# Kernel optimization log

Hardware: AMD Instinct MI355X
Metric: run time of the kernel (lower is better)

The kernel has to match this reference:

```python
import jax, jax.numpy as jnp
import numpy as np

H = 16  # heads
K_POLY = 3  # K from init


def setup_inputs() -> dict:
    key = jax.random.key(0)
    ks = jax.random.split(key, 6)
    B, N, D = 4, 1024, 1024
    s = 1.0 / np.sqrt(D)
    return {
        "x": jax.random.normal(ks[0], (B, N, D), jnp.float32),
        "Wq": jax.random.normal(ks[1], (D, D), jnp.float32) * s,
        "bq": jnp.zeros((D,), jnp.float32),
        "Wk": jax.random.normal(ks[2], (D, D), jnp.float32) * s,
        "bk": jnp.zeros((D,), jnp.float32),
        "Wv": jax.random.normal(ks[3], (D, D), jnp.float32) * s,
        "bv": jnp.zeros((D,), jnp.float32),
        "Wo": jax.random.normal(ks[4], (D, D), jnp.float32) * s,
        "bo": jnp.zeros((D,), jnp.float32),
        "w0": jnp.zeros((H,), jnp.float32),
        "w1": jnp.ones((H,), jnp.float32),
        "wK": jnp.zeros((H,), jnp.float32),
    }


def reference(x, Wq, bq, Wk, bk, Wv, bv, Wo, bo, w0, w1, wK):
    B, N, D = x.shape
    d = D // H
    # projections -> [B, H, N, d]
    def proj(W, b):
        return (x @ W + b).reshape(B, N, H, d).transpose(0, 2, 1, 3)
    q = proj(Wq, bq)
    k = proj(Wk, bk)
    v = proj(Wv, bv)
    att = jax.nn.softmax(jnp.einsum('bhnd,bhmd->bhnm', q, k) / jnp.sqrt(jnp.float32(d)), axis=-1)
    att2 = jnp.einsum('bhnm,bhmk->bhnk', att, att)  # att @ att
    attK = att + (K_POLY - 1) * (att2 - att)
    eye = jnp.eye(N, dtype=x.dtype)  # [N, N]
    gf = (w0[None, :, None, None] * eye[None, None]
          + w1[None, :, None, None] * att
          + wK[None, :, None, None] * attK)
    out = jnp.einsum('bhnm,bhmd->bhnd', gf, v)  # [B, H, N, d]
    out = out.transpose(0, 2, 1, 3).reshape(B, N, D)
    return out @ Wo + bo
```

## Files before the change

### kernel.cpp

```cpp
#include <hip/hip_runtime.h>

typedef unsigned short u16;
typedef unsigned int u32;
typedef __attribute__((ext_vector_type(8))) short short8;
typedef __attribute__((ext_vector_type(4))) float f32x4;

__device__ __forceinline__ u16 f2bf(float f) {
  union { float f; u32 u; } c; c.f = f;
  u32 u = c.u;
  u += 0x7fffu + ((u >> 16) & 1u);
  return (u16)(u >> 16);
}
__device__ __forceinline__ float bf2f(u16 h) {
  union { u32 u; float f; } c; c.u = ((u32)h) << 16;
  return c.f;
}

#define GLDS16(g, l)                                                          \
  __builtin_amdgcn_global_load_lds(                                           \
      (const __attribute__((address_space(1))) u32*)(g),                      \
      (__attribute__((address_space(3))) u32*)(l), 16, 0, 0)

#define EXP_SCALE 0.18033688011112042f

__global__ __launch_bounds__(256) void k_cast_x(const float* __restrict__ x,
                                                u16* __restrict__ xb) {
  int i = blockIdx.x * 256 + threadIdx.x;
  float4 v = ((const float4*)x)[i];
  short4 s;
  s.x = (short)f2bf(v.x); s.y = (short)f2bf(v.y);
  s.z = (short)f2bf(v.z); s.w = (short)f2bf(v.w);
  *(short4*)(xb + (size_t)i * 4) = s;
}

__global__ __launch_bounds__(256) void k_trans_w(
    const float* __restrict__ W0, const float* __restrict__ W1,
    const float* __restrict__ W2, const float* __restrict__ W3,
    u16* __restrict__ T0, u16* __restrict__ T1, u16* __restrict__ T2,
    u16* __restrict__ T3) {
  const float* W = blockIdx.z == 0 ? W0 : blockIdx.z == 1 ? W1 : blockIdx.z == 2 ? W2 : W3;
  u16* T = blockIdx.z == 0 ? T0 : blockIdx.z == 1 ? T1 : blockIdx.z == 2 ? T2 : T3;
  __shared__ float tile[32][33];
  int r0 = blockIdx.y * 32, c0 = blockIdx.x * 32;
  int tid = threadIdx.x;
  for (int i = tid; i < 1024; i += 256) {
    int r = i >> 5, c = i & 31;
    tile[r][c] = W[(size_t)(r0 + r) * 1024 + c0 + c];
  }
  __syncthreads();
  for (int i = tid; i < 1024; i += 256) {
    int r = i >> 5, c = i & 31;
    T[(size_t)(c0 + r) * 1024 + r0 + c] = f2bf(tile[c][r]);
  }
}

__global__ __launch_bounds__(512, 2) void k_proj(
    const u16* __restrict__ xb, const u16* __restrict__ WqT,
    const u16* __restrict__ WkT, const u16* __restrict__ WvT,
    const float* __restrict__ bq, const float* __restrict__ bk,
    const float* __restrict__ bv, u16* __restrict__ qh, u16* __restrict__ kh,
    u16* __restrict__ vh, u16* __restrict__ vT) {
  __shared__ __align__(16) u16 As[3 * 256 * 32];
  __shared__ __align__(16) u16 Bs[3 * 256 * 32];
  const int li = blockIdx.x;
  const int cx = li & 7, j = li >> 3;
  const int g = cx * 24 + j;
  const int which = g >> 6;
  const int rem = g & 63;
  const int n0 = (rem >> 4) * 256;
  const int m0 = (rem & 15) * 256;
  const u16* Ag = xb + (size_t)m0 * 1024;
  const u16* Bg = (which == 0 ? WqT : which == 1 ? WkT : WvT) + (size_t)n0 * 1024;
  const float* bias = which == 0 ? bq : which == 1 ? bk : bv;
  const int tid = threadIdx.x, lane = tid & 63, wid = tid >> 6;
  const int wm = wid >> 2, wn = wid & 3, fr = lane & 15, fg = lane >> 4;

  f32x4 acc[8][4];
#pragma unroll
  for (int i = 0; i < 8; ++i)
#pragma unroll
    for (int jj = 0; jj < 4; ++jj) acc[i][jj] = f32x4{0.f, 0.f, 0.f, 0.f};

  auto stage = [&](int t, int slot) {
    u16* as = As + slot * 8192;
    u16* bs = Bs + slot * 8192;
#pragma unroll
    for (int L = 0; L < 2; ++L) {
      int q = L * 512 + tid;
      int row = q >> 2, c = q & 3;
      GLDS16(Ag + (size_t)row * 1024 + t * 32 + c * 8, as + q * 8);
    }
#pragma unroll
    for (int L = 0; L < 2; ++L) {
      int q = L * 512 + tid;
      int row = q >> 2, c = q & 3;
      GLDS16(Bg + (size_t)row * 1024 + t * 32 + c * 8, bs + q * 8);
    }
  };
  auto compute = [&](int slot) {
    const u16* as = As + slot * 8192;
    const u16* bs = Bs + slot * 8192;
    short8 bf_[4];
#pragma unroll
    for (int jj = 0; jj < 4; ++jj) {
      int row = wn * 64 + jj * 16 + fr;
      bf_[jj] = *(const short8*)(bs + row * 32 + fg * 8);
    }
    short8 af_[8];
#pragma unroll
    for (int i = 0; i < 8; ++i) {
      int row = wm * 128 + i * 16 + fr;
      af_[i] = *(const short8*)(as + row * 32 + fg * 8);
    }
#pragma unroll
    for (int i = 0; i < 8; ++i)
#pragma unroll
      for (int jj = 0; jj < 4; ++jj)
        acc[i][jj] = __builtin_amdgcn_mfma_f32_16x16x32_bf16(af_[i], bf_[jj],
                                                             acc[i][jj], 0, 0, 0);
  };

  const int NS = 32;
  stage(0, 0);
  stage(1, 1);
  int cs = 0, ss = 2;
  for (int t = 0; t + 2 < NS; ++t) {
    asm volatile("s_waitcnt vmcnt(4) lgkmcnt(0)" ::: "memory");
    __builtin_amdgcn_s_barrier();
    asm volatile("" ::: "memory");
    stage(t + 2, ss);
    compute(cs);
    cs = cs == 2 ? 0 : cs + 1;
    ss = ss == 2 ? 0 : ss + 1;
  }
  asm volatile("s_waitcnt vmcnt(4) lgkmcnt(0)" ::: "memory");
  __builtin_amdgcn_s_barrier();
  asm volatile("" ::: "memory");
  compute(cs);
  cs = cs == 2 ? 0 : cs + 1;
  asm volatile("s_waitcnt vmcnt(0) lgkmcnt(0)" ::: "memory");
  __builtin_amdgcn_s_barrier();
  asm volatile("" ::: "memory");
  compute(cs);

#pragma unroll
  for (int f = 0; f < 8; ++f)
#pragma unroll
    for (int j2 = 0; j2 < 4; ++j2) {
      int n = n0 + wn * 64 + j2 * 16 + fr;
      float bb = bias[n];
      int h = n >> 6, dc = n & 63;
#pragma unroll
      for (int r = 0; r < 4; ++r) {
        int m = m0 + wm * 128 + f * 16 + fg * 4 + r;
        int b = m >> 10, nr = m & 1023;
        int z = b * 16 + h;
        float val = acc[f][j2][r] + bb;
        u16 bv16 = f2bf(val);
        if (which == 0) {
          qh[((size_t)z * 1024 + nr) * 64 + dc] = bv16;
        } else if (which == 1) {
          kh[((size_t)z * 1024 + nr) * 64 + dc] = bv16;
        } else {
          vh[((size_t)z * 1024 + nr) * 64 + dc] = bv16;
          vT[((size_t)z * 64 + dc) * 1024 + nr] = bv16;
        }
      }
    }
}

__device__ __forceinline__ void core128x64_p3(const u16* __restrict__ A,
                                              const u16* __restrict__ Bt, int K,
                                              f32x4 (&acc)[2][4], u16* As,
                                              u16* Bs) {
  const int tid = threadIdx.x;
  const int lane = tid & 63;
  const int w = tid >> 6;
  const int fr = lane & 15, fg = lane >> 4;
  const int sr = tid >> 2, sc = (tid & 3) * 8;
#pragma unroll
  for (int i = 0; i < 2; ++i)
#pragma unroll
    for (int j = 0; j < 4; ++j) acc[i][j] = f32x4{0.f, 0.f, 0.f, 0.f};

  auto stage = [&](int t, int slot) {
    u16* as = As + slot * 4096;
    u16* bs = Bs + slot * 2048;
    const int k0 = t * 32 + sc;
    GLDS16(A + (size_t)sr * K + k0, as + tid * 8);
    GLDS16(A + (size_t)(sr + 64) * K + k0, as + (256 + tid) * 8);
    GLDS16(Bt + (size_t)sr * K + k0, bs + tid * 8);
  };
  auto compute = [&](int slot) {
    const u16* as = As + slot * 4096;
    const u16* bs = Bs + slot * 2048;
    short8 af[2], bfv[4];
#pragma unroll
    for (int i = 0; i < 2; ++i)
      af[i] = *(const short8*)(as + (w * 32 + i * 16 + fr) * 32 + fg * 8);
#pragma unroll
    for (int j = 0; j < 4; ++j)
      bfv[j] = *(const short8*)(bs + (j * 16 + fr) * 32 + fg * 8);
#pragma unroll
    for (int i = 0; i < 2; ++i)
#pragma unroll
      for (int j = 0; j < 4; ++j)
        acc[i][j] = __builtin_amdgcn_mfma_f32_16x16x32_bf16(af[i], bfv[j],
                                                            acc[i][j], 0, 0, 0);
  };

  const int NS = K / 32;
  stage(0, 0);
  stage(1, 1);
  int cs = 0, ss = 2;
  for (int t = 0; t + 2 < NS; ++t) {
    asm volatile("s_waitcnt vmcnt(3) lgkmcnt(0)" ::: "memory");
    __builtin_amdgcn_s_barrier();
    asm volatile("" ::: "memory");
    stage(t + 2, ss);
    compute(cs);
    cs = cs == 2 ? 0 : cs + 1;
    ss = ss == 2 ? 0 : ss + 1;
  }
  asm volatile("s_waitcnt vmcnt(3) lgkmcnt(0)" ::: "memory");
  __builtin_amdgcn_s_barrier();
  asm volatile("" ::: "memory");
  compute(cs);
  cs = cs == 2 ? 0 : cs + 1;
  asm volatile("s_waitcnt vmcnt(0) lgkmcnt(0)" ::: "memory");
  __builtin_amdgcn_s_barrier();
  asm volatile("" ::: "memory");
  compute(cs);
}

__global__ __launch_bounds__(256) void k_pass1(
    const u16* __restrict__ qh, const u16* __restrict__ kh,
    const u16* __restrict__ vT, u16* __restrict__ P1T,
    u16* __restrict__ P1h, float* __restrict__ mlinv) {
  __shared__ __align__(16) u16 Ks[64 * 64];
  __shared__ __align__(16) u16 Vs[64 * 64];
  __shared__ __align__(16) u16 Ps[4][16 * 64];
  const int li = blockIdx.x + 16 * blockIdx.y;
  const int cx = li & 7, jb = li >> 3;
  const int z = cx * 8 + (jb >> 4);
  const int m0 = (jb & 15) * 64;
  const int tid = threadIdx.x, lane = tid & 63, w = tid >> 6;
  const int fr = lane & 15, fg = lane >> 4;
  const int row0 = m0 + w * 16;
  const u16* qbase = qh + (size_t)z * 65536;
  const u16* kbase = kh + (size_t)z * 65536;
  const u16* vbase = vT + (size_t)z * 65536;
  u16* myP = &Ps[w][0];

  short8 qf[2];
#pragma unroll
  for (int kc = 0; kc < 2; ++kc)
    qf[kc] = *(const short8*)(qbase + (size_t)(row0 + fr) * 64 + (kc * 4 + fg) * 8);

  f32x4 o[4];
  float rs[4];
#pragma unroll
  for (int ct = 0; ct < 4; ++ct) o[ct] = f32x4{0.f, 0.f, 0.f, 0.f};
#pragma unroll
  for (int r = 0; r < 4; ++r) rs[r] = 0.f;

  for (int t = 0; t < 16; ++t) {
    const int kv0 = t * 64;
#pragma unroll
    for (int it = 0; it < 2; ++it) {
      int idx = it * 256 + tid;
      int row = idx >> 3, cc = idx & 7;
      GLDS16(kbase + (size_t)(kv0 + row) * 64 + ((cc ^ (row & 7)) * 8),
             Ks + idx * 8);
      GLDS16(vbase + (size_t)row * 1024 + kv0 + ((cc ^ (row & 7)) * 8),
             Vs + idx * 8);
    }
    __syncthreads();
#pragma unroll
    for (int ct = 0; ct < 4; ++ct) {
      int krow = ct * 16 + fr;
      short8 k0 = *(const short8*)(Ks + krow * 64 + ((fg ^ (krow & 7)) * 8));
      short8 k1 = *(const short8*)(Ks + krow * 64 + (((4 + fg) ^ (krow & 7)) * 8));
      f32x4 s = __builtin_amdgcn_mfma_f32_16x16x32_bf16(
          qf[0], k0, f32x4{0.f, 0.f, 0.f, 0.f}, 0, 0, 0);
      s = __builtin_amdgcn_mfma_f32_16x16x32_bf16(qf[1], k1, s, 0, 0, 0);
      int pcol = ct * 16 + fr;
      int cc = pcol >> 3;
#pragma unroll
      for (int r = 0; r < 4; ++r) {
        float e = __builtin_exp2f(s[r] * EXP_SCALE);
        rs[r] += e;
        int prow = fg * 4 + r;
        myP[prow * 64 + ((cc ^ (prow & 7)) * 8) + (pcol & 7)] = f2bf(e);
      }
    }
    asm volatile("s_waitcnt lgkmcnt(0)" ::: "memory");
    short8 p0 = *(const short8*)(myP + fr * 64 + ((fg ^ (fr & 7)) * 8));
    short8 p1 = *(const short8*)(myP + fr * 64 + (((4 + fg) ^ (fr & 7)) * 8));
#pragma unroll
    for (int ct = 0; ct < 4; ++ct) {
      int vrow = ct * 16 + fr;
      short8 v0 = *(const short8*)(Vs + vrow * 64 + ((fg ^ (vrow & 7)) * 8));
      short8 v1 = *(const short8*)(Vs + vrow * 64 + (((4 + fg) ^ (vrow & 7)) * 8));
      o[ct] = __builtin_amdgcn_mfma_f32_16x16x32_bf16(p0, v0, o[ct], 0, 0, 0);
      o[ct] = __builtin_amdgcn_mfma_f32_16x16x32_bf16(p1, v1, o[ct], 0, 0, 0);
    }
    __syncthreads();
  }
#pragma unroll
  for (int off = 1; off < 16; off <<= 1)
#pragma unroll
    for (int r = 0; r < 4; ++r) rs[r] += __shfl_xor(rs[r], off, 64);
  float linv[4];
#pragma unroll
  for (int r = 0; r < 4; ++r) linv[r] = 1.f / rs[r];
#pragma unroll
  for (int ct = 0; ct < 4; ++ct) {
    union { u16 u[4]; short4 s4; } pk;
#pragma unroll
    for (int r = 0; r < 4; ++r) {
      u16 b_ = f2bf(o[ct][r] * linv[r]);
      pk.u[r] = b_;
      myP[(fg * 4 + r) * 64 + ct * 16 + fr] = b_;
    }
    *(short4*)(P1T + ((size_t)z * 64 + ct * 16 + fr) * 1024 + row0 + fg * 4) =
        pk.s4;
  }
  asm volatile("s_waitcnt lgkmcnt(0)" ::: "memory");
  {
    int r_ = lane >> 2;
#pragma unroll
    for (int ch2 = 0; ch2 < 2; ++ch2) {
      int ch = (lane & 3) * 2 + ch2;
      int4 vv = *(const int4*)(myP + r_ * 64 + ch * 8);
      *(int4*)(P1h + ((size_t)z * 1024 + row0 + r_) * 64 + ch * 8) = vv;
    }
  }
  if (fr == 0) {
#pragma unroll
    for (int r = 0; r < 4; ++r)
      mlinv[(size_t)z * 1024 + row0 + fg * 4 + r] = linv[r];
  }
}

__global__ __launch_bounds__(256) void k_pass2(
    const u16* __restrict__ qh, const u16* __restrict__ kh,
    const u16* __restrict__ P1T, const u16* __restrict__ vh,
    const u16* __restrict__ P1h, const float* __restrict__ mlinv,
    const float* __restrict__ w0, const float* __restrict__ w1,
    const float* __restrict__ wK, u16* __restrict__ OH) {
  __shared__ __align__(16) u16 Ks[64 * 64];
  __shared__ __align__(16) u16 Ts[64 * 64];
  __shared__ __align__(16) u16 Ps[4][16 * 64];
  const int li = blockIdx.x + 16 * blockIdx.y;
  const int cx = li & 7, jb = li >> 3;
  const int z = cx * 8 + (jb >> 4);
  const int m0 = (jb & 15) * 64;
  const int tid = threadIdx.x, lane = tid & 63, w = tid >> 6;
  const int fr = lane & 15, fg = lane >> 4;
  const int row0 = m0 + w * 16;
  const int h = z & 15, b = z >> 4;
  const float cw0 = w0[h], cw1 = w1[h] - wK[h], cw2 = 2.f * wK[h];
  const u16* qbase = qh + (size_t)z * 65536;
  const u16* kbase = kh + (size_t)z * 65536;
  const u16* tbase = P1T + (size_t)z * 65536;
  u16* myP = &Ps[w][0];

  short8 qf[2];
#pragma unroll
  for (int kc = 0; kc < 2; ++kc)
    qf[kc] = *(const short8*)(qbase + (size_t)(row0 + fr) * 64 + (kc * 4 + fg) * 8);
  float lrow[4];
#pragma unroll
  for (int r = 0; r < 4; ++r)
    lrow[r] = mlinv[(size_t)z * 1024 + row0 + fg * 4 + r];
  f32x4 o[4];
#pragma unroll
  for (int ct = 0; ct < 4; ++ct) o[ct] = f32x4{0.f, 0.f, 0.f, 0.f};

  for (int t = 0; t < 16; ++t) {
    const int kv0 = t * 64;
#pragma unroll
    for (int it = 0; it < 2; ++it) {
      int idx = it * 256 + tid;
      int row = idx >> 3, cc = idx & 7;
      GLDS16(kbase + (size_t)(kv0 + row) * 64 + ((cc ^ (row & 7)) * 8),
             Ks + idx * 8);
      GLDS16(tbase + (size_t)row * 1024 + kv0 + ((cc ^ (row & 7)) * 8),
             Ts + idx * 8);
    }
    __syncthreads();
#pragma unroll
    for (int ct = 0; ct < 4; ++ct) {
      int krow = ct * 16 + fr;
      short8 k0 = *(const short8*)(Ks + krow * 64 + ((fg ^ (krow & 7)) * 8));
      short8 k1 = *(const short8*)(Ks + krow * 64 + (((4 + fg) ^ (krow & 7)) * 8));
      f32x4 s = __builtin_amdgcn_mfma_f32_16x16x32_bf16(
          qf[0], k0, f32x4{0.f, 0.f, 0.f, 0.f}, 0, 0, 0);
      s = __builtin_amdgcn_mfma_f32_16x16x32_bf16(qf[1], k1, s, 0, 0, 0);
      int pcol = ct * 16 + fr;
      int cc = pcol >> 3;
#pragma unroll
      for (int r = 0; r < 4; ++r) {
        float p = __builtin_exp2f(s[r] * EXP_SCALE) * lrow[r];
        int prow = fg * 4 + r;
        myP[prow * 64 + ((cc ^ (prow & 7)) * 8) + (pcol & 7)] = f2bf(p);
      }
    }
    asm volatile("s_waitcnt lgkmcnt(0)" ::: "memory");
    short8 p0 = *(const short8*)(myP + fr * 64 + ((fg ^ (fr & 7)) * 8));
    short8 p1 = *(const short8*)(myP + fr * 64 + (((4 + fg) ^ (fr & 7)) * 8));
#pragma unroll
    for (int ct = 0; ct < 4; ++ct) {
      int vrow = ct * 16 + fr;
      short8 v0 = *(const short8*)(Ts + vrow * 64 + ((fg ^ (vrow & 7)) * 8));
      short8 v1 = *(const short8*)(Ts + vrow * 64 + (((4 + fg) ^ (vrow & 7)) * 8));
      o[ct] = __builtin_amdgcn_mfma_f32_16x16x32_bf16(p0, v0, o[ct], 0, 0, 0);
      o[ct] = __builtin_amdgcn_mfma_f32_16x16x32_bf16(p1, v1, o[ct], 0, 0, 0);
    }
    __syncthreads();
  }
#pragma unroll
  for (int ct = 0; ct < 4; ++ct)
#pragma unroll
    for (int r = 0; r < 4; ++r)
      myP[(fg * 4 + r) * 64 + ct * 16 + fr] = f2bf(o[ct][r]);
  asm volatile("s_waitcnt lgkmcnt(0)" ::: "memory");
  {
    int r_ = lane >> 2;
    const u16* vp = vh + ((size_t)z * 1024 + row0 + r_) * 64;
    const u16* pp = P1h + ((size_t)z * 1024 + row0 + r_) * 64;
    u16* op = OH + ((size_t)b * 1024 + row0 + r_) * 1024 + h * 64;
#pragma unroll
    for (int ch2 = 0; ch2 < 2; ++ch2) {
      int ch = (lane & 3) * 2 + ch2;
      short8 pv = *(const short8*)(myP + r_ * 64 + ch * 8);
      short8 vv = *(const short8*)(vp + ch * 8);
      short8 p1 = *(const short8*)(pp + ch * 8);
      short8 res;
#pragma unroll
      for (int e = 0; e < 8; ++e) {
        float f = cw0 * bf2f((u16)vv[e]) + cw1 * bf2f((u16)p1[e]) +
                  cw2 * bf2f((u16)pv[e]);
        res[e] = (short)f2bf(f);
      }
      *(short8*)(op + ch * 8) = res;
    }
  }
}

__global__ __launch_bounds__(256) void k_final(const u16* __restrict__ OH,
                                               const u16* __restrict__ WoT,
                                               const float* __restrict__ bo,
                                               float* __restrict__ out) {
  __shared__ __align__(16) u16 As[3 * 128 * 32];
  __shared__ __align__(16) u16 Bs[3 * 64 * 32];
  const int li = blockIdx.x + 32 * blockIdx.y;
  const int cx = li & 7, jb = li >> 3;
  const int m0 = (cx * 4 + (jb & 3)) * 128;
  const int n0 = (jb >> 2) * 64;
  f32x4 acc[2][4];
  core128x64_p3(OH + (size_t)m0 * 1024, WoT + (size_t)n0 * 1024, 1024, acc, As, Bs);
  const int tid = threadIdx.x, lane = tid & 63, w = tid >> 6;
  const int fr = lane & 15, fg = lane >> 4;
#pragma unroll
  for (int i = 0; i < 2; ++i)
#pragma unroll
    for (int j2 = 0; j2 < 4; ++j2) {
      int n = n0 + j2 * 16 + fr;
      float bb = bo[n];
#pragma unroll
      for (int r = 0; r < 4; ++r) {
        int m = m0 + w * 32 + i * 16 + fg * 4 + r;
        out[(size_t)m * 1024 + n] = acc[i][j2][r] + bb;
      }
    }
}

extern "C" void kernel_launch(void* const* d_in, const int* in_sizes, int n_in,
                              void* d_out, int out_size, void* d_ws,
                              size_t ws_size, hipStream_t stream) {
  const float* x = (const float*)d_in[0];
  const float* Wq = (const float*)d_in[1];
  const float* bq = (const float*)d_in[2];
  const float* Wk = (const float*)d_in[3];
  const float* bk = (const float*)d_in[4];
  const float* Wv = (const float*)d_in[5];
  const float* bv = (const float*)d_in[6];
  const float* Wo = (const float*)d_in[7];
  const float* bo = (const float*)d_in[8];
  const float* w0 = (const float*)d_in[9];
  const float* w1 = (const float*)d_in[10];
  const float* wK = (const float*)d_in[11];
  float* out = (float*)d_out;

  char* ws = (char*)d_ws;
  const size_t MB = 1ull << 20;
  u16* xb  = (u16*)(ws);
  u16* WqT = (u16*)(ws + 8 * MB);
  u16* WkT = (u16*)(ws + 10 * MB);
  u16* WvT = (u16*)(ws + 12 * MB);
  u16* WoT = (u16*)(ws + 14 * MB);
  u16* qh  = (u16*)(ws + 16 * MB);
  u16* kh  = (u16*)(ws + 24 * MB);
  u16* vh  = (u16*)(ws + 32 * MB);
  u16* vT  = (u16*)(ws + 40 * MB);
  u16* P1T = (u16*)(ws + 48 * MB);
  u16* P1h = (u16*)(ws + 56 * MB);
  u16* OH  = (u16*)(ws + 64 * MB);
  float* mlinv = (float*)(ws + 72 * MB);

  hipLaunchKernelGGL(k_cast_x, dim3(4096), dim3(256), 0, stream, x, xb);
  hipLaunchKernelGGL(k_trans_w, dim3(32, 32, 4), dim3(256), 0, stream, Wq, Wk,
                     Wv, Wo, WqT, WkT, WvT, WoT);
  hipLaunchKernelGGL(k_proj, dim3(192), dim3(512), 0, stream, xb, WqT, WkT,
                     WvT, bq, bk, bv, qh, kh, vh, vT);
  hipLaunchKernelGGL(k_pass1, dim3(16, 64), dim3(256), 0, stream, qh, kh, vT,
                     P1T, P1h, mlinv);
  hipLaunchKernelGGL(k_pass2, dim3(16, 64), dim3(256), 0, stream, qh, kh, P1T,
                     vh, P1h, mlinv, w0, w1, wK, OH);
  hipLaunchKernelGGL(k_final, dim3(32, 16), dim3(256), 0, stream, OH, WoT, bo,
                     out);
}
```

Baseline: 186.9 us.

## Retile projection GEMM and give attention waves two row tiles each

The projection GEMM moves from 512-thread 256x256 tiles with a chiplet-aware block remap to 256-thread 256x128 tiles on a 3D grid. Both attention passes now process 32 query rows per wave (128 rows per block), so each staged K/V (or P1T) tile in shared memory feeds two MFMA row tiles. This halves the K/V traffic per output row and the number of blocks. The cost is half as many blocks in the pass kernels, higher register pressure and loss of the XCD-locality remapping.

```diff
diff --git a/kernel.cpp b/kernel.cpp
--- a/kernel.cpp
+++ b/kernel.cpp
@@ -54,57 +54,52 @@
   }
 }
 
-__global__ __launch_bounds__(512, 2) void k_proj(
+__global__ __launch_bounds__(256) void k_proj(
     const u16* __restrict__ xb, const u16* __restrict__ WqT,
     const u16* __restrict__ WkT, const u16* __restrict__ WvT,
     const float* __restrict__ bq, const float* __restrict__ bk,
     const float* __restrict__ bv, u16* __restrict__ qh, u16* __restrict__ kh,
     u16* __restrict__ vh, u16* __restrict__ vT) {
   __shared__ __align__(16) u16 As[3 * 256 * 32];
-  __shared__ __align__(16) u16 Bs[3 * 256 * 32];
-  const int li = blockIdx.x;
-  const int cx = li & 7, j = li >> 3;
-  const int g = cx * 24 + j;
-  const int which = g >> 6;
-  const int rem = g & 63;
-  const int n0 = (rem >> 4) * 256;
-  const int m0 = (rem & 15) * 256;
+  __shared__ __align__(16) u16 Bs[3 * 128 * 32];
+  const int m0 = blockIdx.x * 256, n0 = blockIdx.y * 128;
+  const int which = blockIdx.z;
   const u16* Ag = xb + (size_t)m0 * 1024;
   const u16* Bg = (which == 0 ? WqT : which == 1 ? WkT : WvT) + (size_t)n0 * 1024;
   const float* bias = which == 0 ? bq : which == 1 ? bk : bv;
-  const int tid = threadIdx.x, lane = tid & 63, wid = tid >> 6;
-  const int wm = wid >> 2, wn = wid & 3, fr = lane & 15, fg = lane >> 4;
+  const int tid = threadIdx.x, lane = tid & 63, w = tid >> 6;
+  const int wm = w >> 1, wn = w & 1, fr = lane & 15, fg = lane >> 4;
 
   f32x4 acc[8][4];
 #pragma unroll
   for (int i = 0; i < 8; ++i)
 #pragma unroll
-    for (int jj = 0; jj < 4; ++jj) acc[i][jj] = f32x4{0.f, 0.f, 0.f, 0.f};
+    for (int j = 0; j < 4; ++j) acc[i][j] = f32x4{0.f, 0.f, 0.f, 0.f};
 
   auto stage = [&](int t, int slot) {
     u16* as = As + slot * 8192;
-    u16* bs = Bs + slot * 8192;
-#pragma unroll
-    for (int L = 0; L < 2; ++L) {
-      int q = L * 512 + tid;
+    u16* bs = Bs + slot * 4096;
+#pragma unroll
+    for (int L = 0; L < 4; ++L) {
+      int q = L * 256 + tid;
       int row = q >> 2, c = q & 3;
       GLDS16(Ag + (size_t)row * 1024 + t * 32 + c * 8, as + q * 8);
     }
 #pragma unroll
     for (int L = 0; L < 2; ++L) {
-      int q = L * 512 + tid;
+      int q = L * 256 + tid;
       int row = q >> 2, c = q & 3;
       GLDS16(Bg + (size_t)row * 1024 + t * 32 + c * 8, bs + q * 8);
     }
   };
   auto compute = [&](int slot) {
     const u16* as = As + slot * 8192;
-    const u16* bs = Bs + slot * 8192;
+    const u16* bs = Bs + slot * 4096;
     short8 bf_[4];
 #pragma unroll
-    for (int jj = 0; jj < 4; ++jj) {
-      int row = wn * 64 + jj * 16 + fr;
-      bf_[jj] = *(const short8*)(bs + row * 32 + fg * 8);
+    for (int j = 0; j < 4; ++j) {
+      int row = wn * 64 + j * 16 + fr;
+      bf_[j] = *(const short8*)(bs + row * 32 + fg * 8);
     }
     short8 af_[8];
 #pragma unroll
@@ -115,9 +110,9 @@
 #pragma unroll
     for (int i = 0; i < 8; ++i)
 #pragma unroll
-      for (int jj = 0; jj < 4; ++jj)
-        acc[i][jj] = __builtin_amdgcn_mfma_f32_16x16x32_bf16(af_[i], bf_[jj],
-                                                             acc[i][jj], 0, 0, 0);
+      for (int j = 0; j < 4; ++j)
+        acc[i][j] = __builtin_amdgcn_mfma_f32_16x16x32_bf16(af_[i], bf_[j],
+                                                            acc[i][j], 0, 0, 0);
   };
 
   const int NS = 32;
@@ -125,7 +120,7 @@
   stage(1, 1);
   int cs = 0, ss = 2;
   for (int t = 0; t + 2 < NS; ++t) {
-    asm volatile("s_waitcnt vmcnt(4) lgkmcnt(0)" ::: "memory");
+    asm volatile("s_waitcnt vmcnt(6) lgkmcnt(0)" ::: "memory");
     __builtin_amdgcn_s_barrier();
     asm volatile("" ::: "memory");
     stage(t + 2, ss);
@@ -133,7 +128,7 @@
     cs = cs == 2 ? 0 : cs + 1;
     ss = ss == 2 ? 0 : ss + 1;
   }
-  asm volatile("s_waitcnt vmcnt(4) lgkmcnt(0)" ::: "memory");
+  asm volatile("s_waitcnt vmcnt(6) lgkmcnt(0)" ::: "memory");
   __builtin_amdgcn_s_barrier();
   asm volatile("" ::: "memory");
   compute(cs);
@@ -239,30 +234,35 @@
     u16* __restrict__ P1h, float* __restrict__ mlinv) {
   __shared__ __align__(16) u16 Ks[64 * 64];
   __shared__ __align__(16) u16 Vs[64 * 64];
-  __shared__ __align__(16) u16 Ps[4][16 * 64];
-  const int li = blockIdx.x + 16 * blockIdx.y;
-  const int cx = li & 7, jb = li >> 3;
-  const int z = cx * 8 + (jb >> 4);
-  const int m0 = (jb & 15) * 64;
+  __shared__ __align__(16) u16 Ps[4][32 * 64];
+  const int z = blockIdx.y;
+  const int m0 = blockIdx.x * 128;
   const int tid = threadIdx.x, lane = tid & 63, w = tid >> 6;
   const int fr = lane & 15, fg = lane >> 4;
-  const int row0 = m0 + w * 16;
+  const int row0 = m0 + w * 32;
   const u16* qbase = qh + (size_t)z * 65536;
   const u16* kbase = kh + (size_t)z * 65536;
   const u16* vbase = vT + (size_t)z * 65536;
   u16* myP = &Ps[w][0];
 
-  short8 qf[2];
-#pragma unroll
-  for (int kc = 0; kc < 2; ++kc)
-    qf[kc] = *(const short8*)(qbase + (size_t)(row0 + fr) * 64 + (kc * 4 + fg) * 8);
-
-  f32x4 o[4];
-  float rs[4];
-#pragma unroll
-  for (int ct = 0; ct < 4; ++ct) o[ct] = f32x4{0.f, 0.f, 0.f, 0.f};
-#pragma unroll
-  for (int r = 0; r < 4; ++r) rs[r] = 0.f;
+  short8 qf[2][2];
+#pragma unroll
+  for (int rt = 0; rt < 2; ++rt)
+#pragma unroll
+    for (int kc = 0; kc < 2; ++kc)
+      qf[rt][kc] = *(const short8*)(qbase + (size_t)(row0 + rt * 16 + fr) * 64 +
+                                    (kc * 4 + fg) * 8);
+
+  f32x4 o[2][4];
+  float rs[2][4];
+#pragma unroll
+  for (int rt = 0; rt < 2; ++rt)
+#pragma unroll
+    for (int ct = 0; ct < 4; ++ct) o[rt][ct] = f32x4{0.f, 0.f, 0.f, 0.f};
+#pragma unroll
+  for (int rt = 0; rt < 2; ++rt)
+#pragma unroll
+    for (int r = 0; r < 4; ++r) rs[rt][r] = 0.f;
 
   for (int t = 0; t < 16; ++t) {
     const int kv0 = t * 64;
@@ -281,65 +281,80 @@
       int krow = ct * 16 + fr;
       short8 k0 = *(const short8*)(Ks + krow * 64 + ((fg ^ (krow & 7)) * 8));
       short8 k1 = *(const short8*)(Ks + krow * 64 + (((4 + fg) ^ (krow & 7)) * 8));
-      f32x4 s = __builtin_amdgcn_mfma_f32_16x16x32_bf16(
-          qf[0], k0, f32x4{0.f, 0.f, 0.f, 0.f}, 0, 0, 0);
-      s = __builtin_amdgcn_mfma_f32_16x16x32_bf16(qf[1], k1, s, 0, 0, 0);
       int pcol = ct * 16 + fr;
       int cc = pcol >> 3;
 #pragma unroll
+      for (int rt = 0; rt < 2; ++rt) {
+        f32x4 s = __builtin_amdgcn_mfma_f32_16x16x32_bf16(
+            qf[rt][0], k0, f32x4{0.f, 0.f, 0.f, 0.f}, 0, 0, 0);
+        s = __builtin_amdgcn_mfma_f32_16x16x32_bf16(qf[rt][1], k1, s, 0, 0, 0);
+#pragma unroll
+        for (int r = 0; r < 4; ++r) {
+          float e = __builtin_exp2f(s[r] * EXP_SCALE);
+          rs[rt][r] += e;
+          int prow = rt * 16 + fg * 4 + r;
+          myP[prow * 64 + ((cc ^ (prow & 7)) * 8) + (pcol & 7)] = f2bf(e);
+        }
+      }
+    }
+    asm volatile("s_waitcnt lgkmcnt(0)" ::: "memory");
+#pragma unroll
+    for (int rt = 0; rt < 2; ++rt) {
+      int prow = rt * 16 + fr;
+      short8 p0 = *(const short8*)(myP + prow * 64 + ((fg ^ (prow & 7)) * 8));
+      short8 p1 = *(const short8*)(myP + prow * 64 + (((4 + fg) ^ (prow & 7)) * 8));
+#pragma unroll
+      for (int ct = 0; ct < 4; ++ct) {
+        int vrow = ct * 16 + fr;
+        short8 v0 = *(const short8*)(Vs + vrow * 64 + ((fg ^ (vrow & 7)) * 8));
+        short8 v1 = *(const short8*)(Vs + vrow * 64 + (((4 + fg) ^ (vrow & 7)) * 8));
+        o[rt][ct] = __builtin_amdgcn_mfma_f32_16x16x32_bf16(p0, v0, o[rt][ct], 0, 0, 0);
+        o[rt][ct] = __builtin_amdgcn_mfma_f32_16x16x32_bf16(p1, v1, o[rt][ct], 0, 0, 0);
+      }
+    }
+    __syncthreads();
+  }
+#pragma unroll
+  for (int off = 1; off < 16; off <<= 1)
+#pragma unroll
+    for (int rt = 0; rt < 2; ++rt)
+#pragma unroll
+      for (int r = 0; r < 4; ++r) rs[rt][r] += __shfl_xor(rs[rt][r], off, 64);
+  float linv[2][4];
+#pragma unroll
+  for (int rt = 0; rt < 2; ++rt)
+#pragma unroll
+    for (int r = 0; r < 4; ++r) linv[rt][r] = 1.f / rs[rt][r];
+#pragma unroll
+  for (int rt = 0; rt < 2; ++rt)
+#pragma unroll
+    for (int ct = 0; ct < 4; ++ct) {
+      union { u16 u[4]; short4 s4; } pk;
+#pragma unroll
       for (int r = 0; r < 4; ++r) {
-        float e = __builtin_exp2f(s[r] * EXP_SCALE);
-        rs[r] += e;
-        int prow = fg * 4 + r;
-        myP[prow * 64 + ((cc ^ (prow & 7)) * 8) + (pcol & 7)] = f2bf(e);
-      }
-    }
-    asm volatile("s_waitcnt lgkmcnt(0)" ::: "memory");
-    short8 p0 = *(const short8*)(myP + fr * 64 + ((fg ^ (fr & 7)) * 8));
-    short8 p1 = *(const short8*)(myP + fr * 64 + (((4 + fg) ^ (fr & 7)) * 8));
-#pragma unroll
-    for (int ct = 0; ct < 4; ++ct) {
-      int vrow = ct * 16 + fr;
-      short8 v0 = *(const short8*)(Vs + vrow * 64 + ((fg ^ (vrow & 7)) * 8));
-      short8 v1 = *(const short8*)(Vs + vrow * 64 + (((4 + fg) ^ (vrow & 7)) * 8));
-      o[ct] = __builtin_amdgcn_mfma_f32_16x16x32_bf16(p0, v0, o[ct], 0, 0, 0);
-      o[ct] = __builtin_amdgcn_mfma_f32_16x16x32_bf16(p1, v1, o[ct], 0, 0, 0);
-    }
-    __syncthreads();
-  }
-#pragma unroll
-  for (int off = 1; off < 16; off <<= 1)
-#pragma unroll
-    for (int r = 0; r < 4; ++r) rs[r] += __shfl_xor(rs[r], off, 64);
-  float linv[4];
-#pragma unroll
-  for (int r = 0; r < 4; ++r) linv[r] = 1.f / rs[r];
-#pragma unroll
-  for (int ct = 0; ct < 4; ++ct) {
-    union { u16 u[4]; short4 s4; } pk;
-#pragma unroll
-    for (int r = 0; r < 4; ++r) {
-      u16 b_ = f2bf(o[ct][r] * linv[r]);
-      pk.u[r] = b_;
-      myP[(fg * 4 + r) * 64 + ct * 16 + fr] = b_;
-    }
-    *(short4*)(P1T + ((size_t)z * 64 + ct * 16 + fr) * 1024 + row0 + fg * 4) =
-        pk.s4;
-  }
+        u16 b_ = f2bf(o[rt][ct][r] * linv[rt][r]);
+        pk.u[r] = b_;
+        myP[(rt * 16 + fg * 4 + r) * 64 + ct * 16 + fr] = b_;
+      }
+      *(short4*)(P1T + ((size_t)z * 64 + ct * 16 + fr) * 1024 + row0 +
+                 rt * 16 + fg * 4) = pk.s4;
+    }
   asm volatile("s_waitcnt lgkmcnt(0)" ::: "memory");
   {
-    int r_ = lane >> 2;
-#pragma unroll
-    for (int ch2 = 0; ch2 < 2; ++ch2) {
-      int ch = (lane & 3) * 2 + ch2;
+    int r_ = lane >> 1, hb = lane & 1;
+#pragma unroll
+    for (int c = 0; c < 4; ++c) {
+      int ch = hb * 4 + c;
       int4 vv = *(const int4*)(myP + r_ * 64 + ch * 8);
       *(int4*)(P1h + ((size_t)z * 1024 + row0 + r_) * 64 + ch * 8) = vv;
     }
   }
   if (fr == 0) {
 #pragma unroll
-    for (int r = 0; r < 4; ++r)
-      mlinv[(size_t)z * 1024 + row0 + fg * 4 + r] = linv[r];
+    for (int rt = 0; rt < 2; ++rt)
+#pragma unroll
+      for (int r = 0; r < 4; ++r)
+        mlinv[(size_t)z * 1024 + row0 + rt * 16 + fg * 4 + r] = linv[rt][r];
   }
 }
 
@@ -351,14 +366,12 @@
     const float* __restrict__ wK, u16* __restrict__ OH) {
   __shared__ __align__(16) u16 Ks[64 * 64];
   __shared__ __align__(16) u16 Ts[64 * 64];
-  __shared__ __align__(16) u16 Ps[4][16 * 64];
-  const int li = blockIdx.x + 16 * blockIdx.y;
-  const int cx = li & 7, jb = li >> 3;
-  const int z = cx * 8 + (jb >> 4);
-  const int m0 = (jb & 15) * 64;
+  __shared__ __align__(16) u16 Ps[4][32 * 64];
+  const int z = blockIdx.y;
+  const int m0 = blockIdx.x * 128;
   const int tid = threadIdx.x, lane = tid & 63, w = tid >> 6;
   const int fr = lane & 15, fg = lane >> 4;
-  const int row0 = m0 + w * 16;
+  const int row0 = m0 + w * 32;
   const int h = z & 15, b = z >> 4;
   const float cw0 = w0[h], cw1 = w1[h] - wK[h], cw2 = 2.f * wK[h];
   const u16* qbase = qh + (size_t)z * 65536;
@@ -366,17 +379,24 @@
   const u16* tbase = P1T + (size_t)z * 65536;
   u16* myP = &Ps[w][0];
 
-  short8 qf[2];
-#pragma unroll
-  for (int kc = 0; kc < 2; ++kc)
-    qf[kc] = *(const short8*)(qbase + (size_t)(row0 + fr) * 64 + (kc * 4 + fg) * 8);
-  float lrow[4];
-#pragma unroll
-  for (int r = 0; r < 4; ++r)
-    lrow[r] = mlinv[(size_t)z * 1024 + row0 + fg * 4 + r];
-  f32x4 o[4];
-#pragma unroll
-  for (int ct = 0; ct < 4; ++ct) o[ct] = f32x4{0.f, 0.f, 0.f, 0.f};
+  short8 qf[2][2];
+#pragma unroll
+  for (int rt = 0; rt < 2; ++rt)
+#pragma unroll
+    for (int kc = 0; kc < 2; ++kc)
+      qf[rt][kc] = *(const short8*)(qbase + (size_t)(row0 + rt * 16 + fr) * 64 +
+                                    (kc * 4 + fg) * 8);
+  float lrow[2][4];
+#pragma unroll
+  for (int rt = 0; rt < 2; ++rt)
+#pragma unroll
+    for (int r = 0; r < 4; ++r)
+      lrow[rt][r] = mlinv[(size_t)z * 1024 + row0 + rt * 16 + fg * 4 + r];
+  f32x4 o[2][4];
+#pragma unroll
+  for (int rt = 0; rt < 2; ++rt)
+#pragma unroll
+    for (int ct = 0; ct < 4; ++ct) o[rt][ct] = f32x4{0.f, 0.f, 0.f, 0.f};
 
   for (int t = 0; t < 16; ++t) {
     const int kv0 = t * 64;
@@ -395,45 +415,54 @@
       int krow = ct * 16 + fr;
       short8 k0 = *(const short8*)(Ks + krow * 64 + ((fg ^ (krow & 7)) * 8));
       short8 k1 = *(const short8*)(Ks + krow * 64 + (((4 + fg) ^ (krow & 7)) * 8));
-      f32x4 s = __builtin_amdgcn_mfma_f32_16x16x32_bf16(
-          qf[0], k0, f32x4{0.f, 0.f, 0.f, 0.f}, 0, 0, 0);
-      s = __builtin_amdgcn_mfma_f32_16x16x32_bf16(qf[1], k1, s, 0, 0, 0);
       int pcol = ct * 16 + fr;
       int cc = pcol >> 3;
 #pragma unroll
-      for (int r = 0; r < 4; ++r) {
-        float p = __builtin_exp2f(s[r] * EXP_SCALE) * lrow[r];
-        int prow = fg * 4 + r;
-        myP[prow * 64 + ((cc ^ (prow & 7)) * 8) + (pcol & 7)] = f2bf(p);
+      for (int rt = 0; rt < 2; ++rt) {
+        f32x4 s = __builtin_amdgcn_mfma_f32_16x16x32_bf16(
+            qf[rt][0], k0, f32x4{0.f, 0.f, 0.f, 0.f}, 0, 0, 0);
+        s = __builtin_amdgcn_mfma_f32_16x16x32_bf16(qf[rt][1], k1, s, 0, 0, 0);
+#pragma unroll
+        for (int r = 0; r < 4; ++r) {
+          float p = __builtin_exp2f(s[r] * EXP_SCALE) * lrow[rt][r];
+          int prow = rt * 16 + fg * 4 + r;
+          myP[prow * 64 + ((cc ^ (prow & 7)) * 8) + (pcol & 7)] = f2bf(p);
+        }
       }
     }
     asm volatile("s_waitcnt lgkmcnt(0)" ::: "memory");
-    short8 p0 = *(const short8*)(myP + fr * 64 + ((fg ^ (fr & 7)) * 8));
-    short8 p1 = *(const short8*)(myP + fr * 64 + (((4 + fg) ^ (fr & 7)) * 8));
-#pragma unroll
-    for (int ct = 0; ct < 4; ++ct) {
-      int vrow = ct * 16 + fr;
-      short8 v0 = *(const short8*)(Ts + vrow * 64 + ((fg ^ (vrow & 7)) * 8));
-      short8 v1 = *(const short8*)(Ts + vrow * 64 + (((4 + fg) ^ (vrow & 7)) * 8));
-      o[ct] = __builtin_amdgcn_mfma_f32_16x16x32_bf16(p0, v0, o[ct], 0, 0, 0);
-      o[ct] = __builtin_amdgcn_mfma_f32_16x16x32_bf16(p1, v1, o[ct], 0, 0, 0);
+#pragma unroll
+    for (int rt = 0; rt < 2; ++rt) {
+      int prow = rt * 16 + fr;
+      short8 p0 = *(const short8*)(myP + prow * 64 + ((fg ^ (prow & 7)) * 8));
+      short8 p1 = *(const short8*)(myP + prow * 64 + (((4 + fg) ^ (prow & 7)) * 8));
+#pragma unroll
+      for (int ct = 0; ct < 4; ++ct) {
+        int vrow = ct * 16 + fr;
+        short8 v0 = *(const short8*)(Ts + vrow * 64 + ((fg ^ (vrow & 7)) * 8));
+        short8 v1 = *(const short8*)(Ts + vrow * 64 + (((4 + fg) ^ (vrow & 7)) * 8));
+        o[rt][ct] = __builtin_amdgcn_mfma_f32_16x16x32_bf16(p0, v0, o[rt][ct], 0, 0, 0);
+        o[rt][ct] = __builtin_amdgcn_mfma_f32_16x16x32_bf16(p1, v1, o[rt][ct], 0, 0, 0);
+      }
     }
     __syncthreads();
   }
 #pragma unroll
-  for (int ct = 0; ct < 4; ++ct)
-#pragma unroll
-    for (int r = 0; r < 4; ++r)
-      myP[(fg * 4 + r) * 64 + ct * 16 + fr] = f2bf(o[ct][r]);
+  for (int rt = 0; rt < 2; ++rt)
+#pragma unroll
+    for (int ct = 0; ct < 4; ++ct)
+#pragma unroll
+      for (int r = 0; r < 4; ++r)
+        myP[(rt * 16 + fg * 4 + r) * 64 + ct * 16 + fr] = f2bf(o[rt][ct][r]);
   asm volatile("s_waitcnt lgkmcnt(0)" ::: "memory");
   {
-    int r_ = lane >> 2;
+    int r_ = lane >> 1, hb = lane & 1;
     const u16* vp = vh + ((size_t)z * 1024 + row0 + r_) * 64;
     const u16* pp = P1h + ((size_t)z * 1024 + row0 + r_) * 64;
     u16* op = OH + ((size_t)b * 1024 + row0 + r_) * 1024 + h * 64;
 #pragma unroll
-    for (int ch2 = 0; ch2 < 2; ++ch2) {
-      int ch = (lane & 3) * 2 + ch2;
+    for (int c = 0; c < 4; ++c) {
+      int ch = hb * 4 + c;
       short8 pv = *(const short8*)(myP + r_ * 64 + ch * 8);
       short8 vv = *(const short8*)(vp + ch * 8);
       short8 p1 = *(const short8*)(pp + ch * 8);
@@ -513,11 +542,11 @@
   hipLaunchKernelGGL(k_cast_x, dim3(4096), dim3(256), 0, stream, x, xb);
   hipLaunchKernelGGL(k_trans_w, dim3(32, 32, 4), dim3(256), 0, stream, Wq, Wk,
                      Wv, Wo, WqT, WkT, WvT, WoT);
-  hipLaunchKernelGGL(k_proj, dim3(192), dim3(512), 0, stream, xb, WqT, WkT,
+  hipLaunchKernelGGL(k_proj, dim3(16, 8, 3), dim3(256), 0, stream, xb, WqT, WkT,
                      WvT, bq, bk, bv, qh, kh, vh, vT);
-  hipLaunchKernelGGL(k_pass1, dim3(16, 64), dim3(256), 0, stream, qh, kh, vT,
+  hipLaunchKernelGGL(k_pass1, dim3(8, 64), dim3(256), 0, stream, qh, kh, vT,
                      P1T, P1h, mlinv);
-  hipLaunchKernelGGL(k_pass2, dim3(16, 64), dim3(256), 0, stream, qh, kh, P1T,
+  hipLaunchKernelGGL(k_pass2, dim3(8, 64), dim3(256), 0, stream, qh, kh, P1T,
                      vh, P1h, mlinv, w0, w1, wK, OH);
   hipLaunchKernelGGL(k_final, dim3(32, 16), dim3(256), 0, stream, OH, WoT, bo,
                      out);
```

New measurement: 186.7 us. No clear change (-0.1%).
